# Performance work log

Measured on AMD Instinct MI355X. Metric: run time of the kernel, lower is better.

Reference implementation:

```python
import jax, jax.numpy as jnp
import numpy as np

D_MODEL = 1024
N_HEADS = 16
D_HEAD = D_MODEL // N_HEADS


def _pid_proj(x, Wp, Wi, Wd, Wg, bg):
    # x: (B, T, D). PID decomposition: proportional / integral (running mean) / derivative (diff).
    T = x.shape[1]
    denom = jnp.arange(1, T + 1, dtype=x.dtype)[None, :, None]
    integral = jnp.cumsum(x, axis=1) / denom
    derivative = jnp.concatenate([jnp.zeros_like(x[:, :1]), x[:, 1:] - x[:, :-1]], axis=1)
    g = jax.nn.softmax(x @ Wg.T + bg, axis=-1)  # (B, T, 3)
    return (g[..., 0:1] * (x @ Wp.T)
            + g[..., 1:2] * (integral @ Wi.T)
            + g[..., 2:3] * (derivative @ Wd.T))


def setup_inputs() -> dict:
    key = jax.random.key(0)
    ks = jax.random.split(key, 16)
    B, T, D = 2, 2048, D_MODEL
    s = 1.0 / np.sqrt(D)

    def lin(k):
        return jax.random.uniform(k, (D, D), jnp.float32, -s, s)

    inp = {"x": jax.random.normal(ks[0], (B, T, D), jnp.float32)}
    names = ["q", "k", "v"]
    i = 1
    for n in names:
        inp[n + "Wp"] = lin(ks[i]); i += 1
        inp[n + "Wi"] = lin(ks[i]) * 0.1; i += 1
        inp[n + "Wd"] = lin(ks[i]) * 0.1; i += 1
        inp[n + "Wg"] = jax.random.uniform(ks[i], (3, D), jnp.float32, -s, s); i += 1
        inp[n + "bg"] = jnp.array([1.0, 0.0, 0.0], jnp.float32)
    inp["oW"] = lin(ks[i]); i += 1
    inp["ob"] = jax.random.uniform(ks[i], (D,), jnp.float32, -s, s)
    return inp


def reference(x, qWp, qWi, qWd, qWg, qbg,
              kWp, kWi, kWd, kWg, kbg,
              vWp, vWi, vWd, vWg, vbg, oW, ob):
    B, T, D = x.shape
    H, dh = N_HEADS, D_HEAD
    Q = _pid_proj(x, qWp, qWi, qWd, qWg, qbg).reshape(B, T, H, dh).transpose(0, 2, 1, 3)
    K = _pid_proj(x, kWp, kWi, kWd, kWg, kbg).reshape(B, T, H, dh).transpose(0, 2, 1, 3)
    V = _pid_proj(x, vWp, vWi, vWd, vWg, vbg).reshape(B, T, H, dh).transpose(0, 2, 1, 3)
    scale = jnp.sqrt(jnp.asarray(dh, x.dtype))
    scores = jnp.einsum('bhqd,bhkd->bhqk', Q, K) / scale  # (B,H,T,T)
    causal = jnp.triu(jnp.ones((T, T), bool), k=1)
    scores = jnp.where(causal[None, None], -jnp.inf, scores)
    attn = jax.nn.softmax(scores, axis=-1)
    out = jnp.einsum('bhqk,bhkd->bhqd', attn, V)
    out = out.transpose(0, 2, 1, 3).reshape(B, T, D)
    return out @ oW.T + ob
```

## Files before the change

### kernel.cpp

```cpp
#include <hip/hip_runtime.h>


#define D_MODEL 1024
#define T_SEQ   2048
#define B_SZ    2
#define M_ROWS  (B_SZ * T_SEQ)
#define N_HEADS 16
#define D_HEAD  64

typedef unsigned short u16;
typedef unsigned int   u32;

typedef short  short8  __attribute__((ext_vector_type(8)));
typedef float  float4v __attribute__((ext_vector_type(4)));

__device__ __forceinline__ float bf2f(u16 u) {
    union { u32 i; float f; } c; c.i = ((u32)u) << 16; return c.f;
}
__device__ __forceinline__ u16 f2bf(float f) {
    union { float f; u32 i; } c; c.f = f;
    u32 i = c.i;
    i += 0x7FFFu + ((i >> 16) & 1u);
    return (u16)(i >> 16);
}
__device__ __forceinline__ float ldin(const void* p, int i, int fl) {
    return fl ? ((const float*)p)[i] : bf2f(((const u16*)p)[i]);
}

__device__ __forceinline__ void glds16(const u16* g, u16* l) {
    __builtin_amdgcn_global_load_lds(
        (const __attribute__((address_space(1))) void*)g,
        (__attribute__((address_space(3))) void*)l, 16, 0, 0);
}

__global__ void detect_kernel(const u32* __restrict__ x, int* __restrict__ flag)
{
    if (threadIdx.x == 0 && blockIdx.x == 0) {
        int good = 0;
        for (int i = 0; i < 256; ++i) {
            union { u32 u; float f; } c; c.u = x[i];
            float a = fabsf(c.f);
            if (c.f == c.f && a > 1e-8f && a < 1e4f) ++good;
        }
        *flag = (good >= 192) ? 1 : 0;
    }
}

__global__ __launch_bounds__(256) void scan_partial(
    const void* __restrict__ x, float* __restrict__ csum,
    const int* __restrict__ flagp)
{
    int fl = *flagp;
    int tid = blockIdx.x * 256 + threadIdx.x;
    int b = tid >> 14;
    int c = (tid >> 10) & 15;
    int d = tid & 1023;
    int base = (b * T_SEQ + c * 128) * D_MODEL + d;
    float s = 0.f;
#pragma unroll 8
    for (int t = 0; t < 128; ++t) s += ldin(x, base + t * D_MODEL, fl);
    csum[tid] = s;
}

__global__ __launch_bounds__(256) void scan_final(
    const void* __restrict__ x, const float* __restrict__ csum,
    u16* __restrict__ integ, const int* __restrict__ flagp)
{
    int fl = *flagp;
    int tid = blockIdx.x * 256 + threadIdx.x;
    int b = tid >> 14;
    int c = (tid >> 10) & 15;
    int d = tid & 1023;
    float pre = 0.f;
    int cbase = (b << 14) | d;
    for (int cc = 0; cc < c; ++cc) pre += csum[cbase + (cc << 10)];
    int base = (b * T_SEQ + c * 128) * D_MODEL + d;
    float run = pre;
    int t0 = c * 128;
    for (int t = 0; t < 128; ++t) {
        run += ldin(x, base + t * D_MODEL, fl);
        integ[base + t * D_MODEL] = f2bf(run / (float)(t0 + t + 1));
    }
}

__global__ __launch_bounds__(64) void gates_kernel(
    const void* __restrict__ x,
    const void* __restrict__ qWg, const void* __restrict__ qbg,
    const void* __restrict__ kWg, const void* __restrict__ kbg,
    const void* __restrict__ vWg, const void* __restrict__ vbg,
    float* __restrict__ gq, float* __restrict__ gk, float* __restrict__ gv,
    const int* __restrict__ flagp)
{
    int fl = *flagp;
    int row = blockIdx.x;
    int l = threadIdx.x;
    int xb = row * D_MODEL;
    float p[9];
#pragma unroll
    for (int j = 0; j < 9; ++j) p[j] = 0.f;
#pragma unroll 4
    for (int i = 0; i < 16; ++i) {
        int d = l + 64 * i;
        float xv = ldin(x, xb + d, fl);
        p[0] += xv * ldin(qWg, d, fl);
        p[1] += xv * ldin(qWg, 1024 + d, fl);
        p[2] += xv * ldin(qWg, 2048 + d, fl);
        p[3] += xv * ldin(kWg, d, fl);
        p[4] += xv * ldin(kWg, 1024 + d, fl);
        p[5] += xv * ldin(kWg, 2048 + d, fl);
        p[6] += xv * ldin(vWg, d, fl);
        p[7] += xv * ldin(vWg, 1024 + d, fl);
        p[8] += xv * ldin(vWg, 2048 + d, fl);
    }
#pragma unroll
    for (int off = 32; off > 0; off >>= 1) {
#pragma unroll
        for (int j = 0; j < 9; ++j) p[j] += __shfl_down(p[j], off);
    }
    if (l == 0) {
        const void* bgs[3] = { qbg, kbg, vbg };
        float* outs[3] = { gq, gk, gv };
#pragma unroll
        for (int pr = 0; pr < 3; ++pr) {
            float a0 = p[pr * 3 + 0] + ldin(bgs[pr], 0, fl);
            float a1 = p[pr * 3 + 1] + ldin(bgs[pr], 1, fl);
            float a2 = p[pr * 3 + 2] + ldin(bgs[pr], 2, fl);
            float mx = fmaxf(a0, fmaxf(a1, a2));
            float e0 = __expf(a0 - mx), e1 = __expf(a1 - mx), e2 = __expf(a2 - mx);
            float inv = 1.f / (e0 + e1 + e2);
            outs[pr][row * 3 + 0] = e0 * inv;
            outs[pr][row * 3 + 1] = e1 * inv;
            outs[pr][row * 3 + 2] = e2 * inv;
        }
    }
}

#define LOFF(row, c) (((((row) >> 4) * 4 + (c)) << 7) + (((row) & 15) << 3))

struct GemmArgs {
    const void* W[3][3];
    const float* G[3];
    u16* C[3];
};

template<int MODE>
__global__ __launch_bounds__(256, 3) void mfma_gemm(
    const void* __restrict__ X, const u16* __restrict__ Ib,
    const u16* __restrict__ Abf, GemmArgs args,
    const void* __restrict__ bias, void* __restrict__ outp,
    const int* __restrict__ flagp, int Ktot)
{
    int fl = *flagp;
    if (fl == 0) return;
    __shared__ __align__(16) u16 As[2 * 4096];
    __shared__ __align__(16) u16 Bs[2 * 4096];

    int tid = threadIdx.x;
    int l = tid & 63, w = tid >> 6;
    int wm = w >> 1, wn = w & 1;
    int m0 = blockIdx.y * 128, n0 = blockIdx.x * 128;
    int z = blockIdx.z;
    int lane15 = l & 15, quad = l >> 4;
    int srow = tid >> 2;
    int cs = tid & 3;
    int skof = cs * 8;

    const void* W0; const void* W1; const void* W2;
    const float* G = nullptr;
    u16* Chead = nullptr;
    if (MODE == 0) {
        W0 = args.W[z][0]; W1 = args.W[z][1]; W2 = args.W[z][2];
        G = args.G[z]; Chead = args.C[z];
    } else {
        W0 = args.W[0][0]; W1 = W0; W2 = W0;
    }

    float gcoef[2][3];
    if (MODE == 0) {
#pragma unroll
        for (int c = 0; c < 2; ++c)
#pragma unroll
            for (int s = 0; s < 3; ++s)
                gcoef[c][s] = G[(m0 + c * 64 + srow) * 3 + s];
    }

    ushort4 ra[2][4];
    ushort4 rb[2][2];

    auto cvt4 = [](float4 t) {
        ushort4 u;
        u.x = f2bf(t.x); u.y = f2bf(t.y); u.z = f2bf(t.z); u.w = f2bf(t.w);
        return u;
    };
    auto ld8 = [&](const void* p, int idx, ushort4& o0, ushort4& o1) {
        if (fl) {
            o0 = cvt4(*(const float4*)((const float*)p + idx));
            o1 = cvt4(*(const float4*)((const float*)p + idx + 4));
        } else {
            o0 = *(const ushort4*)((const u16*)p + idx);
            o1 = *(const ushort4*)((const u16*)p + idx + 4);
        }
    };

    auto load_phase = [&](int k0) {
        int seg = k0 >> 10, ksrc = k0 & 1023;
        const void* Wse = (MODE == 0) ? (seg == 0 ? W0 : (seg == 1 ? W1 : W2)) : W0;
#pragma unroll
        for (int c = 0; c < 2; ++c) {
            int gm = m0 + c * 64 + srow;
            int idx = gm * 1024 + ksrc + skof;
            if (MODE == 1) {
                ra[c][0] = *(const ushort4*)&Abf[idx];
                ra[c][1] = *(const ushort4*)&Abf[idx + 4];
            } else if (seg == 1) {
                ra[c][0] = *(const ushort4*)&Ib[idx];
                ra[c][1] = *(const ushort4*)&Ib[idx + 4];
            } else {
                ld8(X, idx, ra[c][0], ra[c][1]);
                if (seg == 2 && (gm & (T_SEQ - 1)) != 0)
                    ld8(X, idx - 1024, ra[c][2], ra[c][3]);
            }
            int gn = n0 + c * 64 + srow;
            ld8(Wse, gn * 1024 + ksrc + skof, rb[c][0], rb[c][1]);
        }
    };

    auto unp8 = [](ushort4 a, ushort4 b, float v[8]) {
        v[0] = bf2f(a.x); v[1] = bf2f(a.y); v[2] = bf2f(a.z); v[3] = bf2f(a.w);
        v[4] = bf2f(b.x); v[5] = bf2f(b.y); v[6] = bf2f(b.z); v[7] = bf2f(b.w);
    };

    auto store_phase = [&](int k0, int buf) {
        int seg = k0 >> 10;
        u16* Ad = As + buf * 4096;
        u16* Bd = Bs + buf * 4096;
#pragma unroll
        for (int c = 0; c < 2; ++c) {
            int row = c * 64 + srow;
            short8 pk;
            if (MODE == 1) {
                pk[0] = (short)ra[c][0].x; pk[1] = (short)ra[c][0].y;
                pk[2] = (short)ra[c][0].z; pk[3] = (short)ra[c][0].w;
                pk[4] = (short)ra[c][1].x; pk[5] = (short)ra[c][1].y;
                pk[6] = (short)ra[c][1].z; pk[7] = (short)ra[c][1].w;
            } else {
                float v[8];
                unp8(ra[c][0], ra[c][1], v);
                if (seg == 2) {
                    int gm = m0 + row;
                    if ((gm & (T_SEQ - 1)) == 0) {
#pragma unroll
                        for (int j = 0; j < 8; ++j) v[j] = 0.f;
                    } else {
                        float pv[8];
                        unp8(ra[c][2], ra[c][3], pv);
#pragma unroll
                        for (int j = 0; j < 8; ++j) v[j] -= pv[j];
                    }
                }
                float sc = gcoef[c][seg];
#pragma unroll
                for (int j = 0; j < 8; ++j) pk[j] = (short)f2bf(v[j] * sc);
            }
            *(short8*)&Ad[LOFF(row, cs)] = pk;

            short8 pb;
            pb[0] = (short)rb[c][0].x; pb[1] = (short)rb[c][0].y;
            pb[2] = (short)rb[c][0].z; pb[3] = (short)rb[c][0].w;
            pb[4] = (short)rb[c][1].x; pb[5] = (short)rb[c][1].y;
            pb[6] = (short)rb[c][1].z; pb[7] = (short)rb[c][1].w;
            *(short8*)&Bd[LOFF(row, cs)] = pb;
        }
    };

    float4v acc[4][4];
#pragma unroll
    for (int i = 0; i < 4; ++i)
#pragma unroll
        for (int j = 0; j < 4; ++j)
#pragma unroll
            for (int r = 0; r < 4; ++r) acc[i][j][r] = 0.f;

    int nIt = Ktot >> 5;
    load_phase(0);
    store_phase(0, 0);

    for (int it = 0; it < nIt; ++it) {
        __syncthreads();
        int cur = it & 1;
        if (it + 1 < nIt) load_phase((it + 1) << 5);

        short8 af[4], bfr[4];
#pragma unroll
        for (int ms = 0; ms < 4; ++ms)
            af[ms] = *(const short8*)&As[cur * 4096 + ((wm * 4 + ms) * 4 + quad) * 128 + lane15 * 8];
#pragma unroll
        for (int ns = 0; ns < 4; ++ns)
            bfr[ns] = *(const short8*)&Bs[cur * 4096 + ((wn * 4 + ns) * 4 + quad) * 128 + lane15 * 8];
#pragma unroll
        for (int ms = 0; ms < 4; ++ms)
#pragma unroll
            for (int ns = 0; ns < 4; ++ns)
                acc[ms][ns] = __builtin_amdgcn_mfma_f32_16x16x32_bf16(
                    af[ms], bfr[ns], acc[ms][ns], 0, 0, 0);

        if (it + 1 < nIt) store_phase((it + 1) << 5, 1 - cur);
    }

#pragma unroll
    for (int ms = 0; ms < 4; ++ms) {
#pragma unroll
        for (int r = 0; r < 4; ++r) {
            int m = m0 + wm * 64 + ms * 16 + quad * 4 + r;
#pragma unroll
            for (int ns = 0; ns < 4; ++ns) {
                int n = n0 + wn * 64 + ns * 16 + lane15;
                float vv = acc[ms][ns][r];
                if (MODE == 0) {
                    int b = m >> 11, t = m & (T_SEQ - 1);
                    int h = n >> 6,  d = n & 63;
                    Chead[(((b << 4) + h) * T_SEQ + t) * 64 + d] = f2bf(vv);
                } else {
                    vv += ldin(bias, n, fl);
                    if (fl) ((float*)outp)[m * 1024 + n] = vv;
                    else    ((u16*)outp)[m * 1024 + n] = f2bf(vv);
                }
            }
        }
    }
}

template<int MODE>
__global__ __launch_bounds__(256, 3) void fast_gemm(
    const u16* __restrict__ Xb, const u16* __restrict__ Ib,
    GemmArgs args,
    const u16* __restrict__ bias, u16* __restrict__ outp,
    const int* __restrict__ flagp, int Ktot)
{
    if (*flagp != 0) return;

    __shared__ __align__(16) u16 As[2 * 4096];
    __shared__ __align__(16) u16 Bs[2 * 4096];

    int tid = threadIdx.x;
    int l = tid & 63, w = tid >> 6;
    int wm = w >> 1, wn = w & 1;
    int lane15 = l & 15, quad = l >> 4;
    int m0 = blockIdx.x * 128, n0 = blockIdx.y * 128;
    int z = blockIdx.z;

    const u16 *Wp_, *Wi_ = nullptr, *Wd_ = nullptr;
    const float* G = nullptr;
    u16* Chead = nullptr;
    if (MODE == 0) {
        Wp_ = (const u16*)args.W[z][0];
        Wi_ = (const u16*)args.W[z][1];
        Wd_ = (const u16*)args.W[z][2];
        G = args.G[z]; Chead = args.C[z];
    } else {
        Wp_ = (const u16*)args.W[0][0];
    }

    int j0 = w * 2;
    int ri = l & 15;
    int colo = (l >> 4) * 8;

    int mrow0 = m0 + j0 * 16 + ri;
    int mrow1 = mrow0 + 16;
    int nrow0 = n0 + j0 * 16 + ri;
    int nrow1 = nrow0 + 16;

    const u16* pXa0 = Xb + mrow0 * 1024 + colo;
    const u16* pXa1 = Xb + mrow1 * 1024 + colo;
    const u16* pIa0 = nullptr; const u16* pIa1 = nullptr;
    const u16* pPa0 = nullptr; const u16* pPa1 = nullptr;
    if (MODE == 0) {
        pIa0 = Ib + mrow0 * 1024 + colo;
        pIa1 = Ib + mrow1 * 1024 + colo;
        int pr0 = ((mrow0 & (T_SEQ - 1)) == 0) ? mrow0 : mrow0 - 1;
        int pr1 = ((mrow1 & (T_SEQ - 1)) == 0) ? mrow1 : mrow1 - 1;
        pPa0 = Xb + pr0 * 1024 + colo;
        pPa1 = Xb + pr1 * 1024 + colo;
    }

    const u16* pBp0 = Wp_ + nrow0 * 1024 + colo;
    const u16* pBp1 = Wp_ + nrow1 * 1024 + colo;
    const u16* pBi0 = nullptr; const u16* pBi1 = nullptr;
    const u16* pBd0 = nullptr; const u16* pBd1 = nullptr;
    if (MODE == 0) {
        pBi0 = Wi_ + nrow0 * 1024 + colo;
        pBi1 = Wi_ + nrow1 * 1024 + colo;
        pBd0 = Wd_ + nrow0 * 1024 + colo;
        pBd1 = Wd_ + nrow1 * 1024 + colo;
    }

    auto stage = [&](int it, int buf) {
        int kl  = (MODE == 0) ? ((it & 31) << 5) : (it << 5);
        int seg = (MODE == 0) ? (it >> 5) : 0;
        u16* la = As + buf * 4096 + j0 * 512;
        u16* lb = Bs + buf * 4096 + j0 * 512;
        const u16 *a0, *a1, *b0, *b1;
        if (MODE == 1 || seg == 0) {
            a0 = pXa0 + kl; a1 = pXa1 + kl; b0 = pBp0 + kl; b1 = pBp1 + kl;
        } else if (seg == 1) {
            a0 = pIa0 + kl; a1 = pIa1 + kl; b0 = pBi0 + kl; b1 = pBi1 + kl;
        } else if (seg == 2) {
            a0 = pXa0 + kl; a1 = pXa1 + kl; b0 = pBd0 + kl; b1 = pBd1 + kl;
        } else {
            a0 = pPa0 + kl; a1 = pPa1 + kl; b0 = pBd0 + kl; b1 = pBd1 + kl;
        }
        glds16(a0, la);
        glds16(a1, la + 512);
        glds16(b0, lb);
        glds16(b1, lb + 512);
    };

    float4v acc[4][4];
#pragma unroll
    for (int i = 0; i < 4; ++i)
#pragma unroll
        for (int j = 0; j < 4; ++j)
#pragma unroll
            for (int r = 0; r < 4; ++r) acc[i][j][r] = 0.f;

    int nIt = Ktot >> 5;
    stage(0, 0);

    for (int it = 0; it < nIt; ++it) {
        __syncthreads();
        int cur = it & 1;
        if (it + 1 < nIt) stage(it + 1, cur ^ 1);

        if (MODE == 0 && it > 0 && (it & 31) == 0) {
            int s = it >> 5;
#pragma unroll
            for (int ms = 0; ms < 4; ++ms) {
#pragma unroll
                for (int r = 0; r < 4; ++r) {
                    float f;
                    if (s == 3) f = -1.f;
                    else {
                        int row = m0 + wm * 64 + ms * 16 + quad * 4 + r;
                        float ga = G[row * 3 + (s - 1)];
                        float gb = G[row * 3 + s];
                        f = ga / gb;
                    }
#pragma unroll
                    for (int ns = 0; ns < 4; ++ns) acc[ms][ns][r] *= f;
                }
            }
        }

        short8 af[4], bfr[4];
#pragma unroll
        for (int ms = 0; ms < 4; ++ms)
            af[ms] = *(const short8*)&As[cur * 4096 + ((wm * 4 + ms) * 4 + quad) * 128 + lane15 * 8];
#pragma unroll
        for (int ns = 0; ns < 4; ++ns)
            bfr[ns] = *(const short8*)&Bs[cur * 4096 + ((wn * 4 + ns) * 4 + quad) * 128 + lane15 * 8];
#pragma unroll
        for (int ms = 0; ms < 4; ++ms)
#pragma unroll
            for (int ns = 0; ns < 4; ++ns)
                acc[ms][ns] = __builtin_amdgcn_mfma_f32_16x16x32_bf16(
                    af[ms], bfr[ns], acc[ms][ns], 0, 0, 0);
    }

#pragma unroll
    for (int ms = 0; ms < 4; ++ms) {
#pragma unroll
        for (int r = 0; r < 4; ++r) {
            int m = m0 + wm * 64 + ms * 16 + quad * 4 + r;
            float fs = 0.f;
            if (MODE == 0) fs = -G[m * 3 + 2];
#pragma unroll
            for (int ns = 0; ns < 4; ++ns) {
                int n = n0 + wn * 64 + ns * 16 + lane15;
                float vv = acc[ms][ns][r];
                if (MODE == 0) {
                    vv *= fs;
                    int b = m >> 11, t = m & (T_SEQ - 1);
                    int h = n >> 6,  d = n & 63;
                    Chead[(((b << 4) + h) * T_SEQ + t) * 64 + d] = f2bf(vv);
                } else {
                    vv += bf2f(bias[n]);
                    outp[m * 1024 + n] = f2bf(vv);
                }
            }
        }
    }
}

__global__ __launch_bounds__(256) void attn_mfma(
    const u16* __restrict__ Qh, const u16* __restrict__ Kh,
    const u16* __restrict__ Vh, u16* __restrict__ AO)
{
    int bx = blockIdx.x;
    int qt = bx & 31;
    int bh = bx >> 5;
    int h  = bh & 15;
    int b  = bh >> 4;
    int tid = threadIdx.x;
    int l   = tid & 63;
    int w   = tid >> 6;
    int lane15 = l & 15;
    int quad   = l >> 4;

    __shared__ __align__(16) u16 Ks[64 * 72];
    __shared__ __align__(16) u16 Vt[64 * 72];
    __shared__ __align__(16) u16 Ps[4 * 16 * 72];

    const u16* Qb = Qh + bh * (T_SEQ * 64);
    const u16* Kb = Kh + bh * (T_SEQ * 64);
    const u16* Vb = Vh + bh * (T_SEQ * 64);

    int qrow = qt * 64 + w * 16 + lane15;
    short8 qf[2];
#pragma unroll
    for (int ks = 0; ks < 2; ++ks)
        qf[ks] = *(const short8*)&Qb[qrow * 64 + ks * 32 + quad * 8];

    float4v oacc[4];
#pragma unroll
    for (int ds = 0; ds < 4; ++ds)
#pragma unroll
        for (int r = 0; r < 4; ++r) oacc[ds][r] = 0.f;
    float mrun[4], lrun[4];
#pragma unroll
    for (int r = 0; r < 4; ++r) { mrun[r] = -1e30f; lrun[r] = 0.f; }

    int srow = tid >> 2;
    int sdc  = (tid & 3) * 16;

    for (int kt = 0; kt <= qt; ++kt) {
        {
            const u16* kp = &Kb[(kt * 64 + srow) * 64 + sdc];
            ushort4 a = *(const ushort4*)kp;
            ushort4 c = *(const ushort4*)(kp + 4);
            ushort4 d2 = *(const ushort4*)(kp + 8);
            ushort4 e = *(const ushort4*)(kp + 12);
            short8 p0, p1;
            p0[0]=a.x; p0[1]=a.y; p0[2]=a.z; p0[3]=a.w;
            p0[4]=c.x; p0[5]=c.y; p0[6]=c.z; p0[7]=c.w;
            p1[0]=d2.x; p1[1]=d2.y; p1[2]=d2.z; p1[3]=d2.w;
            p1[4]=e.x; p1[5]=e.y; p1[6]=e.z; p1[7]=e.w;
            *(short8*)&Ks[srow * 72 + sdc] = p0;
            *(short8*)&Ks[srow * 72 + sdc + 8] = p1;

            const u16* vp = &Vb[(kt * 64 + srow) * 64 + sdc];
            u16 vv[16];
            *(ushort4*)&vv[0]  = *(const ushort4*)vp;
            *(ushort4*)&vv[4]  = *(const ushort4*)(vp + 4);
            *(ushort4*)&vv[8]  = *(const ushort4*)(vp + 8);
            *(ushort4*)&vv[12] = *(const ushort4*)(vp + 12);
#pragma unroll
            for (int e2 = 0; e2 < 16; ++e2)
                Vt[(sdc + e2) * 72 + srow] = vv[e2];
        }
        __syncthreads();

        float4v sacc[4];
#pragma unroll
        for (int ns = 0; ns < 4; ++ns)
#pragma unroll
            for (int r = 0; r < 4; ++r) sacc[ns][r] = 0.f;
#pragma unroll
        for (int ks = 0; ks < 2; ++ks) {
#pragma unroll
            for (int ns = 0; ns < 4; ++ns) {
                short8 bfk = *(const short8*)&Ks[(ns * 16 + lane15) * 72 + ks * 32 + quad * 8];
                sacc[ns] = __builtin_amdgcn_mfma_f32_16x16x32_bf16(
                    qf[ks], bfk, sacc[ns], 0, 0, 0);
            }
        }

        int qg0 = qt * 64 + w * 16 + quad * 4;
#pragma unroll
        for (int ns = 0; ns < 4; ++ns) {
            int kg = kt * 64 + ns * 16 + lane15;
#pragma unroll
            for (int r = 0; r < 4; ++r) {
                float s = sacc[ns][r] * 0.125f;
                sacc[ns][r] = (kg > qg0 + r) ? -1e30f : s;
            }
        }
#pragma unroll
        for (int r = 0; r < 4; ++r) {
            float mx = fmaxf(fmaxf(sacc[0][r], sacc[1][r]),
                             fmaxf(sacc[2][r], sacc[3][r]));
#pragma unroll
            for (int m2 = 1; m2 < 16; m2 <<= 1)
                mx = fmaxf(mx, __shfl_xor(mx, m2, 64));
            float mnew = fmaxf(mrun[r], mx);
            float al = __expf(mrun[r] - mnew);
            float rs = 0.f;
#pragma unroll
            for (int ns = 0; ns < 4; ++ns) {
                float p = __expf(sacc[ns][r] - mnew);
                sacc[ns][r] = p;
                rs += p;
            }
#pragma unroll
            for (int m2 = 1; m2 < 16; m2 <<= 1)
                rs += __shfl_xor(rs, m2, 64);
            lrun[r] = lrun[r] * al + rs;
            mrun[r] = mnew;
#pragma unroll
            for (int ds = 0; ds < 4; ++ds) oacc[ds][r] *= al;
        }

        u16* Pw = &Ps[w * 16 * 72];
#pragma unroll
        for (int ns = 0; ns < 4; ++ns)
#pragma unroll
            for (int r = 0; r < 4; ++r)
                Pw[(quad * 4 + r) * 72 + ns * 16 + lane15] = f2bf(sacc[ns][r]);

#pragma unroll
        for (int ks = 0; ks < 2; ++ks) {
            short8 afp = *(const short8*)&Pw[lane15 * 72 + ks * 32 + quad * 8];
#pragma unroll
            for (int ds = 0; ds < 4; ++ds) {
                short8 bfv = *(const short8*)&Vt[(ds * 16 + lane15) * 72 + ks * 32 + quad * 8];
                oacc[ds] = __builtin_amdgcn_mfma_f32_16x16x32_bf16(
                    afp, bfv, oacc[ds], 0, 0, 0);
            }
        }
        __syncthreads();
    }

#pragma unroll
    for (int r = 0; r < 4; ++r) {
        float inv = 1.f / lrun[r];
        int t = qt * 64 + w * 16 + quad * 4 + r;
        int orow = (b * T_SEQ + t) * 1024 + h * 64;
#pragma unroll
        for (int ds = 0; ds < 4; ++ds)
            AO[orow + ds * 16 + lane15] = f2bf(oacc[ds][r] * inv);
    }
}

extern "C" void kernel_launch(void* const* d_in, const int* in_sizes, int n_in,
                              void* d_out, int out_size, void* d_ws, size_t ws_size,
                              hipStream_t stream)
{
    const void* x   = d_in[0];
    const void* qWp = d_in[1];
    const void* qWi = d_in[2];
    const void* qWd = d_in[3];
    const void* qWg = d_in[4];
    const void* qbg = d_in[5];
    const void* kWp = d_in[6];
    const void* kWi = d_in[7];
    const void* kWd = d_in[8];
    const void* kWg = d_in[9];
    const void* kbg = d_in[10];
    const void* vWp = d_in[11];
    const void* vWi = d_in[12];
    const void* vWd = d_in[13];
    const void* vWg = d_in[14];
    const void* vbg = d_in[15];
    const void* oW  = d_in[16];
    const void* ob  = d_in[17];

    int*   flag = (int*)d_ws;
    float* fws  = (float*)d_ws;
    float* csum = fws + 64;
    float* gq   = csum + 32768;
    float* gk   = gq + 3 * M_ROWS;
    float* gv   = gk + 3 * M_ROWS;
    const size_t SZ = (size_t)M_ROWS * D_MODEL;
    u16* Ib = (u16*)((char*)d_ws + (1u << 20));
    u16* AO = Ib;
    u16* Qh = Ib + SZ;
    u16* Kh = Qh + SZ;
    u16* Vh = Kh + SZ;

    detect_kernel<<<1, 64, 0, stream>>>((const u32*)x, flag);
    scan_partial<<<128, 256, 0, stream>>>(x, csum, flag);
    scan_final<<<128, 256, 0, stream>>>(x, csum, Ib, flag);
    gates_kernel<<<M_ROWS, 64, 0, stream>>>(x, qWg, qbg, kWg, kbg, vWg, vbg,
                                            gq, gk, gv, flag);

    GemmArgs pa;
    pa.W[0][0] = qWp; pa.W[0][1] = qWi; pa.W[0][2] = qWd;
    pa.W[1][0] = kWp; pa.W[1][1] = kWi; pa.W[1][2] = kWd;
    pa.W[2][0] = vWp; pa.W[2][1] = vWi; pa.W[2][2] = vWd;
    pa.G[0] = gq; pa.G[1] = gk; pa.G[2] = gv;
    pa.C[0] = Qh; pa.C[1] = Kh; pa.C[2] = Vh;

    fast_gemm<0><<<dim3(32, 8, 3), 256, 0, stream>>>(
        (const u16*)x, Ib, pa, nullptr, nullptr, flag, 4096);
    mfma_gemm<0><<<dim3(8, 32, 3), 256, 0, stream>>>(
        x, Ib, nullptr, pa, nullptr, nullptr, flag, 3072);

    attn_mfma<<<B_SZ * N_HEADS * (T_SEQ / 64), 256, 0, stream>>>(Qh, Kh, Vh, AO);

    GemmArgs oa = {};
    oa.W[0][0] = oW;
    fast_gemm<1><<<dim3(32, 8, 1), 256, 0, stream>>>(
        AO, nullptr, oa, (const u16*)ob, (u16*)d_out, flag, 1024);
    mfma_gemm<1><<<dim3(8, 32, 1), 256, 0, stream>>>(
        nullptr, nullptr, AO, oa, ob, d_out, flag, 1024);
}
```

Measured before the change: 596.3 us.

## Precompute bf16 x/derivative and convert weights so fp32 inputs use fast GEMM

The scan kernel now also writes bf16 copies of x and the derivative (x_t - x_{t-1}). A new kernel converts the ten fp32 weight matrices to bf16. The host picks the dtype from the input sizes so the fast bf16 GEMM path handles fp32 inputs too, not only the slower mfma_gemm fallback. The fast GEMM's K is cut from 4096 to 3072 by using the precomputed derivative, the gate scaling is simplified, and the LDS reads are swizzled to reduce bank conflicts. The cost is extra conversion traffic and the use of d_out and workspace as scratch.

```diff
diff --git a/kernel.cpp b/kernel.cpp
--- a/kernel.cpp
+++ b/kernel.cpp
@@ -64,7 +64,8 @@
 
 __global__ __launch_bounds__(256) void scan_final(
     const void* __restrict__ x, const float* __restrict__ csum,
-    u16* __restrict__ integ, const int* __restrict__ flagp)
+    u16* __restrict__ integ, u16* __restrict__ xb, u16* __restrict__ db,
+    const int* __restrict__ flagp)
 {
     int fl = *flagp;
     int tid = blockIdx.x * 256 + threadIdx.x;
@@ -77,9 +78,18 @@
     int base = (b * T_SEQ + c * 128) * D_MODEL + d;
     float run = pre;
     int t0 = c * 128;
+    float xprev = 0.f;
+    if (db != nullptr && c != 0) xprev = ldin(x, base - D_MODEL, fl);
     for (int t = 0; t < 128; ++t) {
-        run += ldin(x, base + t * D_MODEL, fl);
+        float xv = ldin(x, base + t * D_MODEL, fl);
+        run += xv;
         integ[base + t * D_MODEL] = f2bf(run / (float)(t0 + t + 1));
+        if (xb != nullptr) xb[base + t * D_MODEL] = f2bf(xv);
+        if (db != nullptr) {
+            float dv = (t0 + t == 0) ? 0.f : (xv - xprev);
+            db[base + t * D_MODEL] = f2bf(dv);
+            xprev = xv;
+        }
     }
 }
 
@@ -135,6 +145,28 @@
     }
 }
 
+struct CvtArgs { const void* src[10]; };
+
+__global__ __launch_bounds__(256) void cvt_w(CvtArgs a, u16* __restrict__ dst, int fl)
+{
+    int m = blockIdx.y;
+    const void* s = a.src[m];
+    u16* d = dst + (size_t)m * (1u << 20);
+    int i = (blockIdx.x * 256 + threadIdx.x) * 8;
+    if (fl) {
+        float4 v0 = *(const float4*)((const float*)s + i);
+        float4 v1 = *(const float4*)((const float*)s + i + 4);
+        ushort4 o0, o1;
+        o0.x = f2bf(v0.x); o0.y = f2bf(v0.y); o0.z = f2bf(v0.z); o0.w = f2bf(v0.w);
+        o1.x = f2bf(v1.x); o1.y = f2bf(v1.y); o1.z = f2bf(v1.z); o1.w = f2bf(v1.w);
+        *(ushort4*)(d + i) = o0;
+        *(ushort4*)(d + i + 4) = o1;
+    } else {
+        *(ushort4*)(d + i)     = *(const ushort4*)((const u16*)s + i);
+        *(ushort4*)(d + i + 4) = *(const ushort4*)((const u16*)s + i + 4);
+    }
+}
+
 #define LOFF(row, c) (((((row) >> 4) * 4 + (c)) << 7) + (((row) & 15) << 3))
 
 struct GemmArgs {
@@ -151,7 +183,6 @@
     const int* __restrict__ flagp, int Ktot)
 {
     int fl = *flagp;
-    if (fl == 0) return;
     __shared__ __align__(16) u16 As[2 * 4096];
     __shared__ __align__(16) u16 Bs[2 * 4096];
 
@@ -330,15 +361,19 @@
     }
 }
 
+struct FArgs {
+    const u16* W[3][3];
+    const float* G[3];
+    u16* C[3];
+};
+
 template<int MODE>
 __global__ __launch_bounds__(256, 3) void fast_gemm(
     const u16* __restrict__ Xb, const u16* __restrict__ Ib,
-    GemmArgs args,
-    const u16* __restrict__ bias, u16* __restrict__ outp,
-    const int* __restrict__ flagp, int Ktot)
-{
-    if (*flagp != 0) return;
-
+    const u16* __restrict__ Db, FArgs args,
+    const void* __restrict__ bias, void* __restrict__ outp,
+    int fl, int Ktot)
+{
     __shared__ __align__(16) u16 As[2 * 4096];
     __shared__ __align__(16) u16 Bs[2 * 4096];
 
@@ -349,49 +384,35 @@
     int m0 = blockIdx.x * 128, n0 = blockIdx.y * 128;
     int z = blockIdx.z;
 
-    const u16 *Wp_, *Wi_ = nullptr, *Wd_ = nullptr;
+    const u16 *Wp_ = nullptr, *Wi_ = nullptr, *Wd_ = nullptr;
     const float* G = nullptr;
     u16* Chead = nullptr;
     if (MODE == 0) {
-        Wp_ = (const u16*)args.W[z][0];
-        Wi_ = (const u16*)args.W[z][1];
-        Wd_ = (const u16*)args.W[z][2];
+        Wp_ = args.W[z][0]; Wi_ = args.W[z][1]; Wd_ = args.W[z][2];
         G = args.G[z]; Chead = args.C[z];
     } else {
-        Wp_ = (const u16*)args.W[0][0];
+        Wp_ = args.W[0][0];
     }
 
     int j0 = w * 2;
-    int ri = l & 15;
-    int colo = (l >> 4) * 8;
+    int q_s = l >> 4;
+    int ri = ((l & 15) - q_s) & 15;
+    int colo = q_s * 8;
 
     int mrow0 = m0 + j0 * 16 + ri;
-    int mrow1 = mrow0 + 16;
     int nrow0 = n0 + j0 * 16 + ri;
-    int nrow1 = nrow0 + 16;
-
-    const u16* pXa0 = Xb + mrow0 * 1024 + colo;
-    const u16* pXa1 = Xb + mrow1 * 1024 + colo;
-    const u16* pIa0 = nullptr; const u16* pIa1 = nullptr;
-    const u16* pPa0 = nullptr; const u16* pPa1 = nullptr;
+
+    const u16* pXa0 = Xb + (size_t)mrow0 * 1024 + colo;
+    const u16* pXa1 = pXa0 + 16 * 1024;
+    const u16* pBp0 = Wp_ + (size_t)nrow0 * 1024 + colo;
+    const u16* pBp1 = pBp0 + 16 * 1024;
+    const u16 *pIa0 = nullptr, *pIa1 = nullptr, *pDa0 = nullptr, *pDa1 = nullptr;
+    const u16 *pBi0 = nullptr, *pBi1 = nullptr, *pBd0 = nullptr, *pBd1 = nullptr;
     if (MODE == 0) {
-        pIa0 = Ib + mrow0 * 1024 + colo;
-        pIa1 = Ib + mrow1 * 1024 + colo;
-        int pr0 = ((mrow0 & (T_SEQ - 1)) == 0) ? mrow0 : mrow0 - 1;
-        int pr1 = ((mrow1 & (T_SEQ - 1)) == 0) ? mrow1 : mrow1 - 1;
-        pPa0 = Xb + pr0 * 1024 + colo;
-        pPa1 = Xb + pr1 * 1024 + colo;
-    }
-
-    const u16* pBp0 = Wp_ + nrow0 * 1024 + colo;
-    const u16* pBp1 = Wp_ + nrow1 * 1024 + colo;
-    const u16* pBi0 = nullptr; const u16* pBi1 = nullptr;
-    const u16* pBd0 = nullptr; const u16* pBd1 = nullptr;
-    if (MODE == 0) {
-        pBi0 = Wi_ + nrow0 * 1024 + colo;
-        pBi1 = Wi_ + nrow1 * 1024 + colo;
-        pBd0 = Wd_ + nrow0 * 1024 + colo;
-        pBd1 = Wd_ + nrow1 * 1024 + colo;
+        pIa0 = Ib + (size_t)mrow0 * 1024 + colo;  pIa1 = pIa0 + 16 * 1024;
+        pDa0 = Db + (size_t)mrow0 * 1024 + colo;  pDa1 = pDa0 + 16 * 1024;
+        pBi0 = Wi_ + (size_t)nrow0 * 1024 + colo; pBi1 = pBi0 + 16 * 1024;
+        pBd0 = Wd_ + (size_t)nrow0 * 1024 + colo; pBd1 = pBd0 + 16 * 1024;
     }
 
     auto stage = [&](int it, int buf) {
@@ -404,10 +425,8 @@
             a0 = pXa0 + kl; a1 = pXa1 + kl; b0 = pBp0 + kl; b1 = pBp1 + kl;
         } else if (seg == 1) {
             a0 = pIa0 + kl; a1 = pIa1 + kl; b0 = pBi0 + kl; b1 = pBi1 + kl;
-        } else if (seg == 2) {
-            a0 = pXa0 + kl; a1 = pXa1 + kl; b0 = pBd0 + kl; b1 = pBd1 + kl;
         } else {
-            a0 = pPa0 + kl; a1 = pPa1 + kl; b0 = pBd0 + kl; b1 = pBd1 + kl;
+            a0 = pDa0 + kl; a1 = pDa1 + kl; b0 = pBd0 + kl; b1 = pBd1 + kl;
         }
         glds16(a0, la);
         glds16(a1, la + 512);
@@ -426,25 +445,21 @@
     int nIt = Ktot >> 5;
     stage(0, 0);
 
+    int ro = quad * 128 + (((lane15 + quad) & 15) << 3);
+
     for (int it = 0; it < nIt; ++it) {
         __syncthreads();
         int cur = it & 1;
         if (it + 1 < nIt) stage(it + 1, cur ^ 1);
 
-        if (MODE == 0 && it > 0 && (it & 31) == 0) {
+        if (MODE == 0 && (it == 32 || it == 64)) {
             int s = it >> 5;
 #pragma unroll
             for (int ms = 0; ms < 4; ++ms) {
 #pragma unroll
                 for (int r = 0; r < 4; ++r) {
-                    float f;
-                    if (s == 3) f = -1.f;
-                    else {
-                        int row = m0 + wm * 64 + ms * 16 + quad * 4 + r;
-                        float ga = G[row * 3 + (s - 1)];
-                        float gb = G[row * 3 + s];
-                        f = ga / gb;
-                    }
+                    int row = m0 + wm * 64 + ms * 16 + quad * 4 + r;
+                    float f = G[row * 3 + (s - 1)] / G[row * 3 + s];
 #pragma unroll
                     for (int ns = 0; ns < 4; ++ns) acc[ms][ns][r] *= f;
                 }
@@ -454,10 +469,10 @@
         short8 af[4], bfr[4];
 #pragma unroll
         for (int ms = 0; ms < 4; ++ms)
-            af[ms] = *(const short8*)&As[cur * 4096 + ((wm * 4 + ms) * 4 + quad) * 128 + lane15 * 8];
+            af[ms] = *(const short8*)&As[cur * 4096 + (wm * 4 + ms) * 512 + ro];
 #pragma unroll
         for (int ns = 0; ns < 4; ++ns)
-            bfr[ns] = *(const short8*)&Bs[cur * 4096 + ((wn * 4 + ns) * 4 + quad) * 128 + lane15 * 8];
+            bfr[ns] = *(const short8*)&Bs[cur * 4096 + (wn * 4 + ns) * 512 + ro];
 #pragma unroll
         for (int ms = 0; ms < 4; ++ms)
 #pragma unroll
@@ -471,8 +486,8 @@
 #pragma unroll
         for (int r = 0; r < 4; ++r) {
             int m = m0 + wm * 64 + ms * 16 + quad * 4 + r;
-            float fs = 0.f;
-            if (MODE == 0) fs = -G[m * 3 + 2];
+            float fs = 1.f;
+            if (MODE == 0) fs = G[m * 3 + 2];
 #pragma unroll
             for (int ns = 0; ns < 4; ++ns) {
                 int n = n0 + wn * 64 + ns * 16 + lane15;
@@ -483,8 +498,9 @@
                     int h = n >> 6,  d = n & 63;
                     Chead[(((b << 4) + h) * T_SEQ + t) * 64 + d] = f2bf(vv);
                 } else {
-                    vv += bf2f(bias[n]);
-                    outp[m * 1024 + n] = f2bf(vv);
+                    vv += ldin(bias, n, fl);
+                    if (fl) ((float*)outp)[(size_t)m * 1024 + n] = vv;
+                    else    ((u16*)outp)[(size_t)m * 1024 + n] = f2bf(vv);
                 }
             }
         }
@@ -663,43 +679,91 @@
     const void* oW  = d_in[16];
     const void* ob  = d_in[17];
 
+    const size_t SZ = (size_t)M_ROWS * D_MODEL;
+
+    int fl_h = -1;
+    if (in_sizes) {
+        if (in_sizes[0] == (int)(SZ * 4)) fl_h = 1;
+        else if (in_sizes[0] == (int)(SZ * 2)) fl_h = 0;
+    }
+
     int*   flag = (int*)d_ws;
     float* fws  = (float*)d_ws;
     float* csum = fws + 64;
     float* gq   = csum + 32768;
     float* gk   = gq + 3 * M_ROWS;
     float* gv   = gk + 3 * M_ROWS;
-    const size_t SZ = (size_t)M_ROWS * D_MODEL;
     u16* Ib = (u16*)((char*)d_ws + (1u << 20));
     u16* AO = Ib;
     u16* Qh = Ib + SZ;
     u16* Kh = Qh + SZ;
     u16* Vh = Kh + SZ;
+    u16* wb = Vh + SZ;
+
+    size_t need_fast = (1u << 20) + 4 * SZ * 2;
+    if (fl_h == 1) need_fast += 10 * ((size_t)(1u << 20) * 2);
+    bool fast = (fl_h >= 0) && (ws_size >= need_fast);
 
     detect_kernel<<<1, 64, 0, stream>>>((const u32*)x, flag);
     scan_partial<<<128, 256, 0, stream>>>(x, csum, flag);
-    scan_final<<<128, 256, 0, stream>>>(x, csum, Ib, flag);
-    gates_kernel<<<M_ROWS, 64, 0, stream>>>(x, qWg, qbg, kWg, kbg, vWg, vbg,
-                                            gq, gk, gv, flag);
-
-    GemmArgs pa;
-    pa.W[0][0] = qWp; pa.W[0][1] = qWi; pa.W[0][2] = qWd;
-    pa.W[1][0] = kWp; pa.W[1][1] = kWi; pa.W[1][2] = kWd;
-    pa.W[2][0] = vWp; pa.W[2][1] = vWi; pa.W[2][2] = vWd;
-    pa.G[0] = gq; pa.G[1] = gk; pa.G[2] = gv;
-    pa.C[0] = Qh; pa.C[1] = Kh; pa.C[2] = Vh;
-
-    fast_gemm<0><<<dim3(32, 8, 3), 256, 0, stream>>>(
-        (const u16*)x, Ib, pa, nullptr, nullptr, flag, 4096);
-    mfma_gemm<0><<<dim3(8, 32, 3), 256, 0, stream>>>(
-        x, Ib, nullptr, pa, nullptr, nullptr, flag, 3072);
-
-    attn_mfma<<<B_SZ * N_HEADS * (T_SEQ / 64), 256, 0, stream>>>(Qh, Kh, Vh, AO);
-
-    GemmArgs oa = {};
-    oa.W[0][0] = oW;
-    fast_gemm<1><<<dim3(32, 8, 1), 256, 0, stream>>>(
-        AO, nullptr, oa, (const u16*)ob, (u16*)d_out, flag, 1024);
-    mfma_gemm<1><<<dim3(8, 32, 1), 256, 0, stream>>>(
-        nullptr, nullptr, AO, oa, ob, d_out, flag, 1024);
-}
+
+    if (fast) {
+        u16* xb_w = (fl_h == 1) ? (u16*)d_out : nullptr;
+        u16* db   = (fl_h == 1) ? ((u16*)d_out + SZ) : (u16*)d_out;
+        const u16* xb = (fl_h == 1) ? (const u16*)d_out : (const u16*)x;
+
+        scan_final<<<128, 256, 0, stream>>>(x, csum, Ib, xb_w, db, flag);
+        gates_kernel<<<M_ROWS, 64, 0, stream>>>(x, qWg, qbg, kWg, kbg, vWg, vbg,
+                                                gq, gk, gv, flag);
+
+        const void* wsrc[10] = { qWp, qWi, qWd, kWp, kWi, kWd, vWp, vWi, vWd, oW };
+        FArgs fa;
+        const u16* oWb;
+        if (fl_h == 1) {
+            CvtArgs ca;
+            for (int i = 0; i < 10; ++i) ca.src[i] = wsrc[i];
+            cvt_w<<<dim3(512, 10), 256, 0, stream>>>(ca, wb, 1);
+            for (int z2 = 0; z2 < 3; ++z2)
+                for (int s2 = 0; s2 < 3; ++s2)
+                    fa.W[z2][s2] = wb + (size_t)(z2 * 3 + s2) * (1u << 20);
+            oWb = wb + (size_t)9 * (1u << 20);
+        } else {
+            for (int z2 = 0; z2 < 3; ++z2)
+                for (int s2 = 0; s2 < 3; ++s2)
+                    fa.W[z2][s2] = (const u16*)wsrc[z2 * 3 + s2];
+            oWb = (const u16*)oW;
+        }
+        fa.G[0] = gq; fa.G[1] = gk; fa.G[2] = gv;
+        fa.C[0] = Qh; fa.C[1] = Kh; fa.C[2] = Vh;
+
+        fast_gemm<0><<<dim3(32, 8, 3), 256, 0, stream>>>(
+            xb, Ib, db, fa, nullptr, nullptr, fl_h, 3072);
+
+        attn_mfma<<<B_SZ * N_HEADS * (T_SEQ / 64), 256, 0, stream>>>(Qh, Kh, Vh, AO);
+
+        FArgs fo = {};
+        fo.W[0][0] = oWb;
+        fast_gemm<1><<<dim3(32, 8, 1), 256, 0, stream>>>(
+            AO, nullptr, nullptr, fo, ob, d_out, fl_h, 1024);
+    } else {
+        scan_final<<<128, 256, 0, stream>>>(x, csum, Ib, nullptr, nullptr, flag);
+        gates_kernel<<<M_ROWS, 64, 0, stream>>>(x, qWg, qbg, kWg, kbg, vWg, vbg,
+                                                gq, gk, gv, flag);
+
+        GemmArgs pa;
+        pa.W[0][0] = qWp; pa.W[0][1] = qWi; pa.W[0][2] = qWd;
+        pa.W[1][0] = kWp; pa.W[1][1] = kWi; pa.W[1][2] = kWd;
+        pa.W[2][0] = vWp; pa.W[2][1] = vWi; pa.W[2][2] = vWd;
+        pa.G[0] = gq; pa.G[1] = gk; pa.G[2] = gv;
+        pa.C[0] = Qh; pa.C[1] = Kh; pa.C[2] = Vh;
+        mfma_gemm<0><<<dim3(8, 32, 3), 256, 0, stream>>>(
+            x, Ib, nullptr, pa, nullptr, nullptr, flag, 3072);
+
+        attn_mfma<<<B_SZ * N_HEADS * (T_SEQ / 64), 256, 0, stream>>>(Qh, Kh, Vh, AO);
+
+        GemmArgs oa = {};
+        oa.W[0][0] = oW;
+        mfma_gemm<1><<<dim3(8, 32, 1), 256, 0, stream>>>(
+            nullptr, nullptr, AO, oa, ob, d_out, flag, 1024);
+    }
+}
```

New measurement: 639.3 us. 7.2% more time.
